# Optimization experiments

Measured on AMD Instinct MI355X. Metric: run time of the kernel, lower is better.

Reference implementation:

```python
import jax, jax.numpy as jnp
import numpy as np
import math

BLUR = [1.0, 3.0, 3.0, 1.0]
FACTOR = 2


def make_kernel():
    k = jnp.array(BLUR, dtype=jnp.float32)
    k = k[None, :] * k[:, None]
    k = k / k.sum()
    return k * (FACTOR ** 2)  # Upsample scales kernel by factor**2


def setup_inputs() -> dict:
    key = jax.random.key(0)
    k1, k2, k3 = jax.random.split(key, 3)
    B, C, H, W = 8, 512, 128, 128
    inp = jax.random.normal(k1, (B, C, H, W), dtype=jnp.float32)
    skip = jax.random.normal(k2, (B, 3, H // 2, W // 2), dtype=jnp.float32)
    weight = jax.random.normal(k3, (3, C, 3, 3), dtype=jnp.float32)  # EqualConv2d raw weight
    bias = jnp.zeros((3,), dtype=jnp.float32)
    return {"input": inp, "skip": skip, "weight": weight, "bias": bias}


def _upfirdn2d_up2(x, kernel):
    # upfirdn2d(x, kernel, up=2, down=1, pad=(pad0, pad1)) as in StyleGAN2.
    # Zero-stuffing by `factor` then pad (pad0, pad1) then VALID conv with
    # flipped kernel == lax conv with lhs_dilation=factor and right pad
    # extended by (factor-1) (trailing zeros of the stuffed signal).
    kh = kernel.shape[0]
    p = kh - FACTOR
    pad0 = (p + 1) // 2 + FACTOR - 1  # = 2 for k=4, factor=2
    pad1 = p // 2                      # = 1
    C = x.shape[1]
    w = jnp.flip(kernel, (0, 1))[None, None]        # [1,1,kh,kw] (conv, not corr)
    w = jnp.tile(w, (C, 1, 1, 1))                   # depthwise [C,1,kh,kw]
    pad = (pad0, pad1 + FACTOR - 1)
    return jax.lax.conv_general_dilated(
        x, w, window_strides=(1, 1), padding=(pad, pad),
        lhs_dilation=(FACTOR, FACTOR), feature_group_count=C,
        dimension_numbers=("NCHW", "OIHW", "NCHW"))


def reference(input, skip, weight, bias):
    C = input.shape[1]
    scale = 1.0 / math.sqrt(C * 3 * 3)  # equalized-lr scale
    out = jax.lax.conv_general_dilated(
        input, weight * scale, window_strides=(1, 1), padding=((1, 1), (1, 1)),
        dimension_numbers=("NCHW", "OIHW", "NCHW"))
    out = out + bias[None, :, None, None]
    out = out + _upfirdn2d_up2(skip, make_kernel())
    return out
```

## Files before the change

### kernel.cpp

```cpp
#include <hip/hip_runtime.h>
#include <math.h>

#define BATCH 8
#define CIN 512
#define H 128
#define W 128
#define COUT 3
#define CHUNKS 16
#define CH (CIN / CHUNKS)
#define TILE_H 32
#define TILES_Y (H / TILE_H)
#define LROWS (TILE_H + 2)
#define LSTRIDE 132
#define LDS_TILE (LROWS * LSTRIDE + 4)

__global__ __launch_bounds__(256) void torgb_conv(
    const float* __restrict__ in, const float* __restrict__ skip,
    const float* __restrict__ weight, const float* __restrict__ bias,
    float* __restrict__ out)
{
    __shared__ __align__(16) float lds[2][LDS_TILE];
    __shared__ float wlds[COUT * CH * 9];

    const int bx    = blockIdx.x;
    const int tile  = bx & (TILES_Y - 1);
    const int b     = (bx >> 2) & (BATCH - 1);
    const int chunk = bx >> 5;
    const int ci0   = chunk * CH;
    const int y0    = tile * TILE_H;

    const int tid = threadIdx.x;
    const int tx  = tid & (W - 1);
    const int s   = tid >> 7;
    const int py0 = s * 16;

    for (int r = tid; r < LROWS; r += 256) {
        lds[0][r * LSTRIDE + 3] = 0.f;
        lds[0][r * LSTRIDE + LSTRIDE] = 0.f;
        lds[1][r * LSTRIDE + 3] = 0.f;
        lds[1][r * LSTRIDE + LSTRIDE] = 0.f;
    }
    for (int i = tid; i < COUT * CH * 9; i += 256) {
        int co  = i / (CH * 9);
        int rem = i - co * (CH * 9);
        wlds[i] = weight[co * (CIN * 9) + ci0 * 9 + rem];
    }

    const float* inb = in + (size_t)b * CIN * H * W;

    {
        const float4* src = (const float4*)(inb + (size_t)ci0 * H * W);
        for (int i = tid; i < LROWS * (W / 4); i += 256) {
            int r = i >> 5, c4 = i & 31;
            int g = y0 - 1 + r;
            float4 v = make_float4(0.f, 0.f, 0.f, 0.f);
            if (g >= 0 && g < H) v = src[g * (W / 4) + c4];
            *(float4*)&lds[0][r * LSTRIDE + 4 + c4 * 4] = v;
        }
    }

    float acc[16][3];
#pragma unroll
    for (int p = 0; p < 16; p++)
#pragma unroll
        for (int c = 0; c < 3; c++) acc[p][c] = 0.f;

    for (int ci = 0; ci < CH; ci++) {
        __syncthreads();

        const int nxt = ci + 1;
        const bool have = (nxt < CH);
        float4 pre[5];
        int pr[5], pc[5];
        if (have) {
            const float4* src = (const float4*)(inb + (size_t)(ci0 + nxt) * H * W);
#pragma unroll
            for (int k = 0; k < 4; k++) {
                int i = tid + k * 256;
                int r = i >> 5, c4 = i & 31;
                int g = y0 - 1 + r;
                pr[k] = r; pc[k] = c4;
                float4 v = make_float4(0.f, 0.f, 0.f, 0.f);
                if (g >= 0 && g < H) v = src[g * (W / 4) + c4];
                pre[k] = v;
            }
            if (tid < 64) {
                int i = 1024 + tid;
                int r = i >> 5, c4 = i & 31;
                int g = y0 - 1 + r;
                pr[4] = r; pc[4] = c4;
                float4 v = make_float4(0.f, 0.f, 0.f, 0.f);
                if (g >= 0 && g < H) v = src[g * (W / 4) + c4];
                pre[4] = v;
            }
        }

        const float* Bp = &lds[ci & 1][py0 * LSTRIDE + 3 + tx];
        float wv[3][9];
#pragma unroll
        for (int co = 0; co < 3; co++)
#pragma unroll
            for (int k = 0; k < 9; k++)
                wv[co][k] = wlds[(co * CH + ci) * 9 + k];

        float r0[3], r1[3], r2[3];
#pragma unroll
        for (int j = 0; j < 3; j++) { r0[j] = Bp[j]; r1[j] = Bp[LSTRIDE + j]; }
#pragma unroll
        for (int p = 0; p < 16; p++) {
#pragma unroll
            for (int j = 0; j < 3; j++) r2[j] = Bp[(p + 2) * LSTRIDE + j];
#pragma unroll
            for (int co = 0; co < 3; co++)
                acc[p][co] += r0[0] * wv[co][0] + r0[1] * wv[co][1] + r0[2] * wv[co][2]
                            + r1[0] * wv[co][3] + r1[1] * wv[co][4] + r1[2] * wv[co][5]
                            + r2[0] * wv[co][6] + r2[1] * wv[co][7] + r2[2] * wv[co][8];
#pragma unroll
            for (int j = 0; j < 3; j++) { r0[j] = r1[j]; r1[j] = r2[j]; }
        }

        if (have) {
            const int bufi = nxt & 1;
#pragma unroll
            for (int k = 0; k < 4; k++)
                *(float4*)&lds[bufi][pr[k] * LSTRIDE + 4 + pc[k] * 4] = pre[k];
            if (tid < 64)
                *(float4*)&lds[bufi][pr[4] * LSTRIDE + 4 + pc[4] * 4] = pre[4];
        }
    }

    const float scale = 1.0f / sqrtf((float)(CIN * 9));
    float* outb = out + (size_t)b * COUT * H * W;

    int j0, j1; float wh0, wh1;
    if ((tx & 1) == 0) { j0 = tx >> 1;       wh0 = 0.75f; j1 = (tx >> 1) - 1; wh1 = 0.25f; }
    else               { j0 = (tx + 1) >> 1; wh0 = 0.25f; j1 = (tx - 1) >> 1; wh1 = 0.75f; }
    const bool j0ok = (j0 >= 0 && j0 < 64), j1ok = (j1 >= 0 && j1 < 64);

#pragma unroll
    for (int p = 0; p < 16; p++) {
        int y = y0 + py0 + p;
        int i0, i1; float wv0, wv1;
        if ((y & 1) == 0) { i0 = y >> 1;       wv0 = 0.75f; i1 = (y >> 1) - 1; wv1 = 0.25f; }
        else              { i0 = (y + 1) >> 1; wv0 = 0.25f; i1 = (y - 1) >> 1; wv1 = 0.75f; }
        const bool i0ok = (i0 >= 0 && i0 < 64), i1ok = (i1 >= 0 && i1 < 64);
#pragma unroll
        for (int co = 0; co < 3; co++) {
            float v = acc[p][co] * scale;
            if (chunk == 0) {
                const float* sk = skip + (size_t)(b * COUT + co) * 64 * 64;
                float s00 = (i0ok && j0ok) ? sk[i0 * 64 + j0] : 0.f;
                float s01 = (i0ok && j1ok) ? sk[i0 * 64 + j1] : 0.f;
                float s10 = (i1ok && j0ok) ? sk[i1 * 64 + j0] : 0.f;
                float s11 = (i1ok && j1ok) ? sk[i1 * 64 + j1] : 0.f;
                v += bias[co] + wv0 * (wh0 * s00 + wh1 * s01)
                              + wv1 * (wh0 * s10 + wh1 * s11);
            }
            atomicAdd(&outb[(size_t)co * H * W + y * W + tx], v);
        }
    }
}

extern "C" void kernel_launch(void* const* d_in, const int* in_sizes, int n_in,
                              void* d_out, int out_size, void* d_ws, size_t ws_size,
                              hipStream_t stream) {
    const float* in     = (const float*)d_in[0];
    const float* skip   = (const float*)d_in[1];
    const float* weight = (const float*)d_in[2];
    const float* bias   = (const float*)d_in[3];
    float* out = (float*)d_out;

    hipMemsetAsync(out, 0, (size_t)out_size * sizeof(float), stream);
    dim3 grid(CHUNKS * BATCH * TILES_Y);
    torgb_conv<<<grid, 256, 0, stream>>>(in, skip, weight, bias, out);
}
```

Before: 426.8 us.

## Replace LDS tiling with register-resident rows and wave shuffles for halo

Drops the shared-memory double buffer and block-wide syncs. Each wave now owns 8 output rows, each lane holds two adjacent columns per row in registers, and the horizontal halo comes from cross-lane shuffles. Input is prefetched into register buffers one channel ahead, and weights are read straight from global memory instead of LDS. Channel chunks double to 32, which doubles the grid and the number of atomic adds per output, and raises register pressure.

```diff
diff --git a/kernel.cpp b/kernel.cpp
--- a/kernel.cpp
+++ b/kernel.cpp
@@ -6,157 +6,153 @@
 #define H 128
 #define W 128
 #define COUT 3
-#define CHUNKS 16
+#define CHUNKS 32
 #define CH (CIN / CHUNKS)
-#define TILE_H 32
-#define TILES_Y (H / TILE_H)
-#define LROWS (TILE_H + 2)
-#define LSTRIDE 132
-#define LDS_TILE (LROWS * LSTRIDE + 4)
+#define R 8
+#define NROWS (R + 2)
+#define WAVES 4
+#define BLOCK_ROWS (R * WAVES)
+#define TILES_Y (H / BLOCK_ROWS)
+
+__device__ __forceinline__ void compute_ch(
+    const float2 (&cur)[NROWS], const float* __restrict__ wp,
+    float (&acc)[R][2][3], int lane, float m0, float m9)
+{
+    float wv[27];
+#pragma unroll
+    for (int co = 0; co < 3; co++)
+#pragma unroll
+        for (int k = 0; k < 9; k++)
+            wv[co * 9 + k] = wp[co * (CIN * 9) + k];
+
+    float lw[3], ax[3], ay[3], rw[3];
+#pragma unroll
+    for (int rr = 0; rr < NROWS; rr++) {
+        const int s = rr % 3;
+        float vx = cur[rr].x, vy = cur[rr].y;
+        if (rr == 0)         { vx *= m0; vy *= m0; }
+        if (rr == NROWS - 1) { vx *= m9; vy *= m9; }
+        float l = __shfl_up(vy, 1);
+        float r_ = __shfl_down(vx, 1);
+        lw[s] = (lane == 0)  ? 0.f : l;
+        rw[s] = (lane == 63) ? 0.f : r_;
+        ax[s] = vx; ay[s] = vy;
+
+        if (rr >= 2) {
+            const int p  = rr - 2;
+            const int s0 = p % 3, s1 = (p + 1) % 3, s2 = (p + 2) % 3;
+#pragma unroll
+            for (int co = 0; co < 3; co++) {
+                const float* w = &wv[co * 9];
+                float a0 = acc[p][0][co], a1 = acc[p][1][co];
+                a0 += lw[s0] * w[0] + ax[s0] * w[1] + ay[s0] * w[2];
+                a1 += ax[s0] * w[0] + ay[s0] * w[1] + rw[s0] * w[2];
+                a0 += lw[s1] * w[3] + ax[s1] * w[4] + ay[s1] * w[5];
+                a1 += ax[s1] * w[3] + ay[s1] * w[4] + rw[s1] * w[5];
+                a0 += lw[s2] * w[6] + ax[s2] * w[7] + ay[s2] * w[8];
+                a1 += ax[s2] * w[6] + ay[s2] * w[7] + rw[s2] * w[8];
+                acc[p][0][co] = a0; acc[p][1][co] = a1;
+            }
+        }
+    }
+}
+
+__device__ __forceinline__ void prefetch_ch(
+    float2 (&buf)[NROWS], const float* __restrict__ chan,
+    const int (&goff)[NROWS], int x0)
+{
+#pragma unroll
+    for (int r = 0; r < NROWS; r++)
+        buf[r] = *(const float2*)(chan + goff[r] + x0);
+}
 
 __global__ __launch_bounds__(256) void torgb_conv(
     const float* __restrict__ in, const float* __restrict__ skip,
     const float* __restrict__ weight, const float* __restrict__ bias,
     float* __restrict__ out)
 {
-    __shared__ __align__(16) float lds[2][LDS_TILE];
-    __shared__ float wlds[COUT * CH * 9];
-
     const int bx    = blockIdx.x;
     const int tile  = bx & (TILES_Y - 1);
     const int b     = (bx >> 2) & (BATCH - 1);
     const int chunk = bx >> 5;
     const int ci0   = chunk * CH;
-    const int y0    = tile * TILE_H;
 
-    const int tid = threadIdx.x;
-    const int tx  = tid & (W - 1);
-    const int s   = tid >> 7;
-    const int py0 = s * 16;
+    const int tid  = threadIdx.x;
+    const int lane = tid & 63;
+    const int wave = tid >> 6;
+    const int yb   = tile * BLOCK_ROWS + wave * R;
+    const int x0   = 2 * lane;
 
-    for (int r = tid; r < LROWS; r += 256) {
-        lds[0][r * LSTRIDE + 3] = 0.f;
-        lds[0][r * LSTRIDE + LSTRIDE] = 0.f;
-        lds[1][r * LSTRIDE + 3] = 0.f;
-        lds[1][r * LSTRIDE + LSTRIDE] = 0.f;
+    int goff[NROWS];
+#pragma unroll
+    for (int r = 0; r < NROWS; r++) {
+        int g = yb - 1 + r;
+        int gc = g < 0 ? 0 : (g > H - 1 ? H - 1 : g);
+        goff[r] = gc * W;
     }
-    for (int i = tid; i < COUT * CH * 9; i += 256) {
-        int co  = i / (CH * 9);
-        int rem = i - co * (CH * 9);
-        wlds[i] = weight[co * (CIN * 9) + ci0 * 9 + rem];
-    }
+    const float m0 = (yb >= 1) ? 1.f : 0.f;
+    const float m9 = (yb + R <= H - 1) ? 1.f : 0.f;
 
-    const float* inb = in + (size_t)b * CIN * H * W;
+    float acc[R][2][3];
+#pragma unroll
+    for (int p = 0; p < R; p++)
+#pragma unroll
+        for (int q = 0; q < 2; q++)
+#pragma unroll
+            for (int c = 0; c < 3; c++) acc[p][q][c] = 0.f;
 
-    {
-        const float4* src = (const float4*)(inb + (size_t)ci0 * H * W);
-        for (int i = tid; i < LROWS * (W / 4); i += 256) {
-            int r = i >> 5, c4 = i & 31;
-            int g = y0 - 1 + r;
-            float4 v = make_float4(0.f, 0.f, 0.f, 0.f);
-            if (g >= 0 && g < H) v = src[g * (W / 4) + c4];
-            *(float4*)&lds[0][r * LSTRIDE + 4 + c4 * 4] = v;
-        }
-    }
+    const float* chan0 = in + ((size_t)b * CIN + ci0) * H * W;
+    const float* wbase = weight + (size_t)ci0 * 9;
 
-    float acc[16][3];
-#pragma unroll
-    for (int p = 0; p < 16; p++)
-#pragma unroll
-        for (int c = 0; c < 3; c++) acc[p][c] = 0.f;
+    float2 bufA[NROWS], bufB[NROWS];
+    prefetch_ch(bufA, chan0, goff, x0);
 
-    for (int ci = 0; ci < CH; ci++) {
-        __syncthreads();
-
-        const int nxt = ci + 1;
-        const bool have = (nxt < CH);
-        float4 pre[5];
-        int pr[5], pc[5];
-        if (have) {
-            const float4* src = (const float4*)(inb + (size_t)(ci0 + nxt) * H * W);
-#pragma unroll
-            for (int k = 0; k < 4; k++) {
-                int i = tid + k * 256;
-                int r = i >> 5, c4 = i & 31;
-                int g = y0 - 1 + r;
-                pr[k] = r; pc[k] = c4;
-                float4 v = make_float4(0.f, 0.f, 0.f, 0.f);
-                if (g >= 0 && g < H) v = src[g * (W / 4) + c4];
-                pre[k] = v;
-            }
-            if (tid < 64) {
-                int i = 1024 + tid;
-                int r = i >> 5, c4 = i & 31;
-                int g = y0 - 1 + r;
-                pr[4] = r; pc[4] = c4;
-                float4 v = make_float4(0.f, 0.f, 0.f, 0.f);
-                if (g >= 0 && g < H) v = src[g * (W / 4) + c4];
-                pre[4] = v;
-            }
-        }
-
-        const float* Bp = &lds[ci & 1][py0 * LSTRIDE + 3 + tx];
-        float wv[3][9];
-#pragma unroll
-        for (int co = 0; co < 3; co++)
-#pragma unroll
-            for (int k = 0; k < 9; k++)
-                wv[co][k] = wlds[(co * CH + ci) * 9 + k];
-
-        float r0[3], r1[3], r2[3];
-#pragma unroll
-        for (int j = 0; j < 3; j++) { r0[j] = Bp[j]; r1[j] = Bp[LSTRIDE + j]; }
-#pragma unroll
-        for (int p = 0; p < 16; p++) {
-#pragma unroll
-            for (int j = 0; j < 3; j++) r2[j] = Bp[(p + 2) * LSTRIDE + j];
-#pragma unroll
-            for (int co = 0; co < 3; co++)
-                acc[p][co] += r0[0] * wv[co][0] + r0[1] * wv[co][1] + r0[2] * wv[co][2]
-                            + r1[0] * wv[co][3] + r1[1] * wv[co][4] + r1[2] * wv[co][5]
-                            + r2[0] * wv[co][6] + r2[1] * wv[co][7] + r2[2] * wv[co][8];
-#pragma unroll
-            for (int j = 0; j < 3; j++) { r0[j] = r1[j]; r1[j] = r2[j]; }
-        }
-
-        if (have) {
-            const int bufi = nxt & 1;
-#pragma unroll
-            for (int k = 0; k < 4; k++)
-                *(float4*)&lds[bufi][pr[k] * LSTRIDE + 4 + pc[k] * 4] = pre[k];
-            if (tid < 64)
-                *(float4*)&lds[bufi][pr[4] * LSTRIDE + 4 + pc[4] * 4] = pre[4];
-        }
+#pragma unroll 2
+    for (int ci = 0; ci < CH; ci += 2) {
+        prefetch_ch(bufB, chan0 + (size_t)(ci + 1) * H * W, goff, x0);
+        compute_ch(bufA, wbase + (size_t)ci * 9, acc, lane, m0, m9);
+        if (ci + 2 < CH)
+            prefetch_ch(bufA, chan0 + (size_t)(ci + 2) * H * W, goff, x0);
+        compute_ch(bufB, wbase + (size_t)(ci + 1) * 9, acc, lane, m0, m9);
     }
 
     const float scale = 1.0f / sqrtf((float)(CIN * 9));
     float* outb = out + (size_t)b * COUT * H * W;
 
-    int j0, j1; float wh0, wh1;
-    if ((tx & 1) == 0) { j0 = tx >> 1;       wh0 = 0.75f; j1 = (tx >> 1) - 1; wh1 = 0.25f; }
-    else               { j0 = (tx + 1) >> 1; wh0 = 0.25f; j1 = (tx - 1) >> 1; wh1 = 0.75f; }
-    const bool j0ok = (j0 >= 0 && j0 < 64), j1ok = (j1 >= 0 && j1 < 64);
+    int j0[2], j1[2]; float wh0[2], wh1[2]; bool j0ok[2], j1ok[2];
+#pragma unroll
+    for (int q = 0; q < 2; q++) {
+        int x = x0 + q;
+        if ((x & 1) == 0) { j0[q] = x >> 1;       wh0[q] = 0.75f; j1[q] = (x >> 1) - 1; wh1[q] = 0.25f; }
+        else              { j0[q] = (x + 1) >> 1; wh0[q] = 0.25f; j1[q] = (x - 1) >> 1; wh1[q] = 0.75f; }
+        j0ok[q] = (j0[q] >= 0 && j0[q] < 64);
+        j1ok[q] = (j1[q] >= 0 && j1[q] < 64);
+    }
 
 #pragma unroll
-    for (int p = 0; p < 16; p++) {
-        int y = y0 + py0 + p;
+    for (int p = 0; p < R; p++) {
+        int y = yb + p;
         int i0, i1; float wv0, wv1;
         if ((y & 1) == 0) { i0 = y >> 1;       wv0 = 0.75f; i1 = (y >> 1) - 1; wv1 = 0.25f; }
         else              { i0 = (y + 1) >> 1; wv0 = 0.25f; i1 = (y - 1) >> 1; wv1 = 0.75f; }
         const bool i0ok = (i0 >= 0 && i0 < 64), i1ok = (i1 >= 0 && i1 < 64);
 #pragma unroll
-        for (int co = 0; co < 3; co++) {
-            float v = acc[p][co] * scale;
-            if (chunk == 0) {
-                const float* sk = skip + (size_t)(b * COUT + co) * 64 * 64;
-                float s00 = (i0ok && j0ok) ? sk[i0 * 64 + j0] : 0.f;
-                float s01 = (i0ok && j1ok) ? sk[i0 * 64 + j1] : 0.f;
-                float s10 = (i1ok && j0ok) ? sk[i1 * 64 + j0] : 0.f;
-                float s11 = (i1ok && j1ok) ? sk[i1 * 64 + j1] : 0.f;
-                v += bias[co] + wv0 * (wh0 * s00 + wh1 * s01)
-                              + wv1 * (wh0 * s10 + wh1 * s11);
+        for (int q = 0; q < 2; q++) {
+            int x = x0 + q;
+#pragma unroll
+            for (int co = 0; co < 3; co++) {
+                float v = acc[p][q][co] * scale;
+                if (chunk == 0) {
+                    const float* sk = skip + (size_t)(b * COUT + co) * 64 * 64;
+                    float s00 = (i0ok && j0ok[q]) ? sk[i0 * 64 + j0[q]] : 0.f;
+                    float s01 = (i0ok && j1ok[q]) ? sk[i0 * 64 + j1[q]] : 0.f;
+                    float s10 = (i1ok && j0ok[q]) ? sk[i1 * 64 + j0[q]] : 0.f;
+                    float s11 = (i1ok && j1ok[q]) ? sk[i1 * 64 + j1[q]] : 0.f;
+                    v += bias[co] + wv0 * (wh0[q] * s00 + wh1[q] * s01)
+                                  + wv1 * (wh0[q] * s10 + wh1[q] * s11);
+                }
+                atomicAdd(&outb[(size_t)co * H * W + y * W + x], v);
             }
-            atomicAdd(&outb[(size_t)co * H * W + y * W + tx], v);
         }
     }
 }
```

After: 432.1 us. Within noise of the previous version (+1.2%).
